# Kernel optimization log

Measured on AMD Instinct MI355X. Metric: run time of the kernel, lower is better.

Reference implementation:

```python
import jax, jax.numpy as jnp
import numpy as np

N_USER = 25000
N_ITEM = 25000
N = N_USER + N_ITEM
E = 1_250_000
D = 64
L = 3
B = 4096


def setup_inputs() -> dict:
    key = jax.random.key(0)
    ks = jax.random.split(key, 11)
    emb = jax.random.normal(ks[0], (N, D), dtype=jnp.float32) * 0.1
    w1_w = jax.random.normal(ks[1], (L, D, D), dtype=jnp.float32) / np.sqrt(D)
    w1_b = jax.random.normal(ks[2], (L, D), dtype=jnp.float32) * 0.01
    w2_w = jax.random.normal(ks[3], (L, D, D), dtype=jnp.float32) / np.sqrt(D)
    w2_b = jax.random.normal(ks[4], (L, D), dtype=jnp.float32) * 0.01
    # normalized-laplacian-like nonneg values
    vals = jax.random.uniform(ks[5], (E,), dtype=jnp.float32) * 0.1
    rows = jax.random.randint(ks[6], (E,), 0, N, dtype=jnp.int32)
    cols = jax.random.randint(ks[7], (E,), 0, N, dtype=jnp.int32)
    user = jax.random.randint(ks[8], (B,), 0, N_USER, dtype=jnp.int32)
    pos = jax.random.randint(ks[9], (B,), 0, N, dtype=jnp.int32)
    neg = jax.random.randint(ks[10], (B,), 0, N, dtype=jnp.int32)
    return {"emb": emb, "w1_w": w1_w, "w1_b": w1_b, "w2_w": w2_w,
            "w2_b": w2_b, "vals": vals, "rows": rows, "cols": cols,
            "user": user, "pos": pos, "neg": neg}


def _spmm(vals, rows, cols, x):
    # sparse [N,N] @ dense [N,D] via gather + segment_sum
    msg = vals[:, None] * x[cols]          # [E, D]
    return jax.ops.segment_sum(msg, rows, num_segments=N)  # [N, D]


def reference(emb, w1_w, w1_b, w2_w, w2_b, vals, rows, cols, user, pos, neg):
    user_embs = [emb[user]]
    pos_embs = [emb[pos]]
    neg_embs = [emb[neg]]
    for l in range(L):
        agg = _spmm(vals, rows, cols, emb)                # sp.mm(laplacian, emb)
        # (laplacian + identity) @ emb == agg + emb
        sx = (agg + emb) @ w1_w[l].T + w1_b[l]
        ox = agg * (emb @ w2_w[l].T + w2_b[l])
        emb = jax.nn.leaky_relu(sx + ox, negative_slope=0.01)
        user_embs.append(emb[user])
        pos_embs.append(emb[pos])
        neg_embs.append(emb[neg])
    user_e = jnp.concatenate(user_embs, axis=-1)          # [B, (L+1)*D]
    pos_e = jnp.concatenate(pos_embs, axis=-1)
    neg_e = jnp.concatenate(neg_embs, axis=-1)
    pos_logits = jnp.einsum('id,id->i', user_e, pos_e)
    neg_logits = jnp.einsum('id,id->i', user_e, neg_e)
    # -log(sigmoid(diff)).sum(), computed stably
    return -jnp.sum(jax.nn.log_sigmoid(pos_logits - neg_logits))
```

## Files before the change

kernel.cpp:

```cpp
#include <hip/hip_runtime.h>
#include <hip/hip_fp16.h>
#include <math.h>

#define N_NODES 50000
#define EDGES   1250000
#define DIM     64
#define NLAYER  3
#define BATCH   4096
#define NSLOTS  (3 * BATCH)

#define NBUCK 196
#define RPB   256
#define NABLK 512
#define CAP_S 7424
#define BCAP  CAP_S
#define PER_BLK ((EDGES + NABLK - 1) / NABLK)

typedef unsigned int uint32;
typedef _Float16 f16x8 __attribute__((ext_vector_type(8)));
typedef float f32x4 __attribute__((ext_vector_type(4)));

static __device__ __forceinline__ ushort f2h(float f) {
    return __half_as_ushort(__float2half(f));
}
static __device__ __forceinline__ float h2f(ushort u) {
    return __half2float(__ushort_as_half(u));
}

static __device__ __forceinline__ int slot_node(int slot,
                                                const int* __restrict__ user,
                                                const int* __restrict__ pos,
                                                const int* __restrict__ neg) {
    if (slot < BATCH) return user[slot];
    if (slot < 2 * BATCH) return pos[slot - BATCH];
    return neg[slot - 2 * BATCH];
}


#define SP_F2H   512
#define SP_DOTS  3637
#define SP_TOTAL 4661

__global__ __launch_bounds__(256) void scatterprep_kernel(const int* __restrict__ rows,
                                                          const int* __restrict__ cols,
                                                          const float* __restrict__ vals,
                                                          int* __restrict__ gcur,
                                                          int2* __restrict__ staging,
                                                          const float* __restrict__ emb,
                                                          ushort* __restrict__ xh,
                                                          const int* __restrict__ user,
                                                          const int* __restrict__ pos,
                                                          const int* __restrict__ neg,
                                                          float* __restrict__ dots,
                                                          float* __restrict__ out) {
    __shared__ int2 sedge[PER_BLK];
    __shared__ int h[NBUCK];
    __shared__ int roff[NBUCK];
    int blk = blockIdx.x;
    int tid = threadIdx.x;
    if (blk < SP_F2H) {
        if (blk == 0 && tid == 0) out[0] = 0.f;
        for (int i = tid; i < NBUCK; i += 256) h[i] = 0;
        __syncthreads();
        int e0 = blk * PER_BLK;
        int e1 = min(e0 + PER_BLK, EDGES);
        int cnt = e1 - e0;
        for (int i = tid; i < cnt; i += 256) {
            int e = e0 + i;
            int r = rows[e];
            sedge[i] = make_int2((r << 16) | cols[e], __float_as_int(vals[e]));
            atomicAdd(&h[r >> 8], 1);
        }
        __syncthreads();
        for (int t = tid; t < NBUCK; t += 256)
            roff[t] = t * CAP_S + atomicAdd(&gcur[t], h[t]);
        __syncthreads();
        for (int i = tid; i < cnt; i += 256) {
            int2 e = sedge[i];
            int bkt = ((uint32)e.x) >> 24;
            int p = atomicAdd(&roff[bkt], 1);
            if (p < (bkt + 1) * CAP_S)
                staging[p] = make_int2(e.x & 0x00FFFFFF, e.y);
        }
    } else if (blk < SP_DOTS) {
        int i = (blk - SP_F2H) * 256 + tid;
        float4 v = ((const float4*)emb)[i];
        ushort4 hh;
        hh.x = f2h(v.x); hh.y = f2h(v.y); hh.z = f2h(v.z); hh.w = f2h(v.w);
        ((ushort4*)xh)[i] = hh;
    } else {
        int lane = tid & 63;
        int i = (blk - SP_DOTS) * 4 + (tid >> 6);
        int ui = user[i], pi = pos[i], ni = neg[i];
        float u = emb[(size_t)ui * DIM + lane];
        float p = emb[(size_t)pi * DIM + lane];
        float n = emb[(size_t)ni * DIM + lane];
        float v = u * (p - n);
#pragma unroll
        for (int off = 32; off; off >>= 1) v += __shfl_xor(v, off);
        if (lane == 0) dots[i] = v;
    }
}


__global__ __launch_bounds__(512) void csr_build_kernel(const int* __restrict__ gcur,
                                                        const int2* __restrict__ staging,
                                                        int* __restrict__ row_ptr,
                                                        uint32* __restrict__ csr) {
    __shared__ int2 sedge[BCAP];
    __shared__ int sbase[256];
    __shared__ int rcur[RPB];
    __shared__ int wred[4];
    int b = blockIdx.x;
    int tid = threadIdx.x;
    int lane = tid & 63, wid = tid >> 6;

    int tot = (tid < NBUCK) ? gcur[tid] : 0;
    int sB = tot;
    if (tid < 256) {
#pragma unroll
        for (int off = 1; off < 64; off <<= 1) {
            int tt = __shfl_up(sB, off);
            if (lane >= off) sB += tt;
        }
        if (lane == 63) wred[wid] = sB;
    }
    __syncthreads();
    if (tid == 0) {
        int a = 0;
#pragma unroll
        for (int i = 0; i < 4; ++i) { int tt = wred[i]; wred[i] = a; a += tt; }
    }
    __syncthreads();
    if (tid < 256) sbase[tid] = wred[wid] + sB - tot;
    __syncthreads();
    int base = sbase[b];
    int cnt = (b == NBUCK - 1) ? (EDGES - sbase[NBUCK - 1]) : (sbase[b + 1] - sbase[b]);
    int sbeg = b * CAP_S;
    __syncthreads();

    if (tid < RPB) rcur[tid] = 0;
    __syncthreads();
    for (int p = tid; p < cnt; p += 512) {
        int2 e = staging[sbeg + p];
        sedge[p] = e;
        atomicAdd(&rcur[e.x >> 16], 1);
    }
    __syncthreads();
    int v = 0, s = 0;
    if (tid < RPB) {
        v = rcur[tid];
        s = v;
#pragma unroll
        for (int off = 1; off < 64; off <<= 1) {
            int t = __shfl_up(s, off);
            if (lane >= off) s += t;
        }
        if (lane == 63) wred[wid] = s;
    }
    __syncthreads();
    if (tid == 0) {
        int a = 0;
#pragma unroll
        for (int i = 0; i < 4; ++i) { int t = wred[i]; wred[i] = a; a += t; }
    }
    __syncthreads();
    if (tid < RPB) {
        int excl = wred[wid] + s - v;
        rcur[tid] = base + excl;
        int row = b * RPB + tid;
        if (row < N_NODES) row_ptr[row] = base + excl;
    }
    if (b == NBUCK - 1 && tid == 0) row_ptr[N_NODES] = EDGES;
    __syncthreads();
    for (int p = tid; p < cnt; p += 512) {
        int2 e = sedge[p];
        int pos = atomicAdd(&rcur[e.x >> 16], 1);
        csr[pos] = ((uint32)(e.x & 0xFFFF) << 16) | (uint32)f2h(__int_as_float(e.y));
    }
}


static __device__ __forceinline__ void spmm_row(const uint32* __restrict__ csr,
                                                const ushort* __restrict__ xh,
                                                int p0, int p1, int g, int sl,
                                                float* a) {
#define SPMM_ACC(E, X)                                                     \
    {                                                                      \
        float vv = h2f((ushort)((E) & 0xFFFF));                            \
        a[0] += vv * h2f((ushort)((X).x & 0xFFFF));                        \
        a[1] += vv * h2f((ushort)((X).x >> 16));                           \
        a[2] += vv * h2f((ushort)((X).y & 0xFFFF));                        \
        a[3] += vv * h2f((ushort)((X).y >> 16));                           \
        a[4] += vv * h2f((ushort)((X).z & 0xFFFF));                        \
        a[5] += vv * h2f((ushort)((X).z >> 16));                           \
        a[6] += vv * h2f((ushort)((X).w & 0xFFFF));                        \
        a[7] += vv * h2f((ushort)((X).w >> 16));                           \
    }
    int p = p0;
    for (; p + 32 <= p1; p += 32) {
        uint32 e0 = csr[p + g];
        uint32 e1 = csr[p + 8 + g];
        uint32 e2 = csr[p + 16 + g];
        uint32 e3 = csr[p + 24 + g];
        uint4 x0 = *(const uint4*)(xh + (size_t)(e0 >> 16) * DIM + sl * 8);
        uint4 x1 = *(const uint4*)(xh + (size_t)(e1 >> 16) * DIM + sl * 8);
        uint4 x2 = *(const uint4*)(xh + (size_t)(e2 >> 16) * DIM + sl * 8);
        uint4 x3 = *(const uint4*)(xh + (size_t)(e3 >> 16) * DIM + sl * 8);
        SPMM_ACC(e0, x0);
        SPMM_ACC(e1, x1);
        SPMM_ACC(e2, x2);
        SPMM_ACC(e3, x3);
    }
    for (; p + 8 <= p1; p += 8) {
        uint32 ea = csr[p + g];
        uint4 xa = *(const uint4*)(xh + (size_t)(ea >> 16) * DIM + sl * 8);
        SPMM_ACC(ea, xa);
    }
    if (p + g < p1) {
        uint32 ea = csr[p + g];
        uint4 xa = *(const uint4*)(xh + (size_t)(ea >> 16) * DIM + sl * 8);
        SPMM_ACC(ea, xa);
    }
#undef SPMM_ACC
#pragma unroll
    for (int m = 8; m <= 32; m <<= 1) {
        a[0] += __shfl_xor(a[0], m); a[1] += __shfl_xor(a[1], m);
        a[2] += __shfl_xor(a[2], m); a[3] += __shfl_xor(a[3], m);
        a[4] += __shfl_xor(a[4], m); a[5] += __shfl_xor(a[5], m);
        a[6] += __shfl_xor(a[6], m); a[7] += __shfl_xor(a[7], m);
    }
}

static __device__ __forceinline__ void spmm_store(ushort* dst, const float* a, int lane) {
    if (lane < 8) {
        ushort t[8];
        t[0] = f2h(a[0]); t[1] = f2h(a[1]); t[2] = f2h(a[2]); t[3] = f2h(a[3]);
        t[4] = f2h(a[4]); t[5] = f2h(a[5]); t[6] = f2h(a[6]); t[7] = f2h(a[7]);
        *(uint4*)(dst + lane * 8) = *(uint4*)t;
    }
}

static __device__ __forceinline__ void dots_tail(const ushort* __restrict__ xh,
                                                 const int* __restrict__ user,
                                                 const int* __restrict__ pos,
                                                 const int* __restrict__ neg,
                                                 float* __restrict__ dots,
                                                 int i, int lane) {
    int ui = user[i], pi = pos[i], ni = neg[i];
    float u = h2f(xh[(size_t)ui * DIM + lane]);
    float p = h2f(xh[(size_t)pi * DIM + lane]);
    float n = h2f(xh[(size_t)ni * DIM + lane]);
    float v = u * (p - n);
#pragma unroll
    for (int off = 32; off; off >>= 1) v += __shfl_xor(v, off);
    if (lane == 0) dots[i] = v;
}


__global__ __launch_bounds__(256) void spmm_kernel(const int* __restrict__ row_ptr,
                                                   const uint32* __restrict__ csr,
                                                   const ushort* __restrict__ xh,
                                                   ushort* __restrict__ aggh,
                                                   const int* __restrict__ user,
                                                   const int* __restrict__ pos,
                                                   const int* __restrict__ neg,
                                                   float* __restrict__ dots,
                                                   int nsb) {
    int lane = threadIdx.x & 63;
    if ((int)blockIdx.x >= nsb) {
        int i = (blockIdx.x - nsb) * 4 + (threadIdx.x >> 6);
        dots_tail(xh, user, pos, neg, dots, i, lane);
        return;
    }
    int row = blockIdx.x * 4 + (threadIdx.x >> 6);
    int p0 = row_ptr[row], p1 = row_ptr[row + 1];
    float a[8] = {};
    spmm_row(csr, xh, p0, p1, lane >> 3, lane & 7, a);
    spmm_store(aggh + (size_t)row * DIM, a, lane);
}


__global__ __launch_bounds__(256) void spmm_slots_kernel(const int* __restrict__ row_ptr,
                                                         const uint32* __restrict__ csr,
                                                         const ushort* __restrict__ xh,
                                                         ushort* __restrict__ aggh_slot,
                                                         const int* __restrict__ user,
                                                         const int* __restrict__ pos,
                                                         const int* __restrict__ neg,
                                                         float* __restrict__ dots,
                                                         int nsb) {
    int lane = threadIdx.x & 63;
    if ((int)blockIdx.x >= nsb) {
        int i = (blockIdx.x - nsb) * 4 + (threadIdx.x >> 6);
        dots_tail(xh, user, pos, neg, dots, i, lane);
        return;
    }
    int slot = blockIdx.x * 4 + (threadIdx.x >> 6);
    int node = slot_node(slot, user, pos, neg);
    int p0 = row_ptr[node], p1 = row_ptr[node + 1];
    float a[8] = {};
    spmm_row(csr, xh, p0, p1, lane >> 3, lane & 7, a);
    spmm_store(aggh_slot + (size_t)slot * DIM, a, lane);
}


template <int IS_SLOT>
static __device__ __forceinline__ void dense_body(const ushort* __restrict__ xh_in,
                                                  const ushort* __restrict__ aggh,
                                                  const float* __restrict__ w1,
                                                  const float* __restrict__ w2,
                                                  const float* __restrict__ b1,
                                                  const float* __restrict__ b2,
                                                  ushort* __restrict__ yh,
                                                  const int* __restrict__ user,
                                                  const int* __restrict__ pos,
                                                  const int* __restrict__ neg) {
    __shared__ ushort xs[64 * 64];
    __shared__ ushort xc[64 * 64];
    __shared__ ushort w1s[64 * 64];
    __shared__ ushort w2s[64 * 64];

    int tid = threadIdx.x;
    int n0 = blockIdx.x * 64;

    {
        int rr = tid >> 2;
        int jq = (tid & 3) << 4;
        int sw = rr & 7;
        int b0 = jq >> 3;
        int o0 = rr * 64 + (((b0 + 0) ^ sw) << 3);
        int o1 = rr * 64 + (((b0 + 1) ^ sw) << 3);

        {
            const float* w1r = w1 + rr * 64 + jq;
            const float* w2r = w2 + rr * 64 + jq;
            ushort t1[16], t2[16];
#pragma unroll
            for (int k = 0; k < 4; ++k) {
                float4 a = ((const float4*)w1r)[k];
                float4 b = ((const float4*)w2r)[k];
                t1[k * 4 + 0] = f2h(a.x); t1[k * 4 + 1] = f2h(a.y);
                t1[k * 4 + 2] = f2h(a.z); t1[k * 4 + 3] = f2h(a.w);
                t2[k * 4 + 0] = f2h(b.x); t2[k * 4 + 1] = f2h(b.y);
                t2[k * 4 + 2] = f2h(b.z); t2[k * 4 + 3] = f2h(b.w);
            }
            *(uint4*)&w1s[o0] = *(uint4*)&t1[0];
            *(uint4*)&w1s[o1] = *(uint4*)&t1[8];
            *(uint4*)&w2s[o0] = *(uint4*)&t2[0];
            *(uint4*)&w2s[o1] = *(uint4*)&t2[8];
        }
        {
            int rowid = n0 + rr;
            int xnode, arow;
            if (IS_SLOT) {
                xnode = slot_node(rowid, user, pos, neg);
                arow = rowid;
            } else {
                xnode = (rowid < N_NODES) ? rowid : (N_NODES - 1);
                arow = xnode;
            }
            const ushort* ar = aggh + (size_t)arow * DIM + jq;
            const ushort* xr = xh_in + (size_t)xnode * DIM + jq;
            ushort txs[16], txc[16];
#pragma unroll
            for (int k = 0; k < 2; ++k) {
                uint4 xv = ((const uint4*)xr)[k];
                uint4 av = ((const uint4*)ar)[k];
                uint32 xw[4] = {xv.x, xv.y, xv.z, xv.w};
                uint32 aw[4] = {av.x, av.y, av.z, av.w};
#pragma unroll
                for (int q = 0; q < 4; ++q) {
                    ushort xlo = (ushort)(xw[q] & 0xFFFF);
                    ushort xhi = (ushort)(xw[q] >> 16);
                    ushort alo = (ushort)(aw[q] & 0xFFFF);
                    ushort ahi = (ushort)(aw[q] >> 16);
                    int e = k * 8 + q * 2;
                    txc[e] = xlo; txc[e + 1] = xhi;
                    txs[e] = f2h(h2f(xlo) + h2f(alo));
                    txs[e + 1] = f2h(h2f(xhi) + h2f(ahi));
                }
            }
            *(uint4*)&xs[o0] = *(uint4*)&txs[0];
            *(uint4*)&xs[o1] = *(uint4*)&txs[8];
            *(uint4*)&xc[o0] = *(uint4*)&txc[0];
            *(uint4*)&xc[o1] = *(uint4*)&txc[8];
        }
    }
    __syncthreads();

    int lane = tid & 63, w = tid >> 6;
    int nb = w << 4;
    int lm = lane & 15;
    int le = lane >> 4;

    f16x8 axs[2], axc[2];
#pragma unroll
    for (int k = 0; k < 2; ++k) {
        int n = nb + lm;
        int blk = k * 4 + le;
        int off = n * 64 + ((blk ^ (n & 7)) << 3);
        axs[k] = *(const f16x8*)&xs[off];
        axc[k] = *(const f16x8*)&xc[off];
    }

#pragma unroll
    for (int dt = 0; dt < 4; ++dt) {
        int d = dt * 16 + lm;
        f16x8 bf1[2], bf2[2];
#pragma unroll
        for (int k = 0; k < 2; ++k) {
            int blk = k * 4 + le;
            int off = d * 64 + ((blk ^ (d & 7)) << 3);
            bf1[k] = *(const f16x8*)&w1s[off];
            bf2[k] = *(const f16x8*)&w2s[off];
        }
        f32x4 acc1 = {0.f, 0.f, 0.f, 0.f};
        f32x4 acc2 = {0.f, 0.f, 0.f, 0.f};
        acc1 = __builtin_amdgcn_mfma_f32_16x16x32_f16(axs[0], bf1[0], acc1, 0, 0, 0);
        acc1 = __builtin_amdgcn_mfma_f32_16x16x32_f16(axs[1], bf1[1], acc1, 0, 0, 0);
        acc2 = __builtin_amdgcn_mfma_f32_16x16x32_f16(axc[0], bf2[0], acc2, 0, 0, 0);
        acc2 = __builtin_amdgcn_mfma_f32_16x16x32_f16(axc[1], bf2[1], acc2, 0, 0, 0);

        float b1v = b1[d], b2v = b2[d];
        int bb = d >> 3;
#pragma unroll
        for (int i = 0; i < 4; ++i) {
            int nl = nb + (le << 2) + i;
            int rowid = n0 + nl;
            int off = nl * 64 + ((bb ^ (nl & 7)) << 3) + (d & 7);
            float ag = h2f(xs[off]) - h2f(xc[off]);
            float t = acc1[i] + b1v + ag * (acc2[i] + b2v);
            t = (t > 0.f) ? t : 0.01f * t;
            bool wr = IS_SLOT ? true : (rowid < N_NODES);
            if (wr) yh[(size_t)rowid * DIM + d] = f2h(t);
        }
    }
}

__global__ __launch_bounds__(256) void dense_kernel(const ushort* __restrict__ xh_in,
                                                    const ushort* __restrict__ aggh,
                                                    const float* __restrict__ w1,
                                                    const float* __restrict__ w2,
                                                    const float* __restrict__ b1,
                                                    const float* __restrict__ b2,
                                                    ushort* __restrict__ yh) {
    dense_body<0>(xh_in, aggh, w1, w2, b1, b2, yh, nullptr, nullptr, nullptr);
}

__global__ __launch_bounds__(256) void dense_slots_kernel(const ushort* __restrict__ xh_in,
                                                          const ushort* __restrict__ aggh_slot,
                                                          const float* __restrict__ w1,
                                                          const float* __restrict__ w2,
                                                          const float* __restrict__ b1,
                                                          const float* __restrict__ b2,
                                                          ushort* __restrict__ yh_slot,
                                                          const int* __restrict__ user,
                                                          const int* __restrict__ pos,
                                                          const int* __restrict__ neg) {
    dense_body<1>(xh_in, aggh_slot, w1, w2, b1, b2, yh_slot, user, pos, neg);
}


__global__ __launch_bounds__(256) void dots_loss_kernel(const ushort* __restrict__ yh_slot,
                                                        const float* __restrict__ dots,
                                                        float* __restrict__ out) {
    __shared__ float part[4];
    int tid = threadIdx.x;
    int lane = tid & 63;
    int i = blockIdx.x * 4 + (tid >> 6);
    float u = h2f(yh_slot[(size_t)i * DIM + lane]);
    float p = h2f(yh_slot[(size_t)(BATCH + i) * DIM + lane]);
    float n = h2f(yh_slot[(size_t)(2 * BATCH + i) * DIM + lane]);
    float v = u * (p - n);
#pragma unroll
    for (int off = 32; off; off >>= 1) v += __shfl_xor(v, off);
    if (lane == 0) {
        float d = dots[i] + dots[BATCH + i] + dots[2 * BATCH + i] + v;
        part[tid >> 6] = fmaxf(-d, 0.f) + log1pf(expf(-fabsf(d)));
    }
    __syncthreads();
    if (tid == 0) atomicAdd(out, part[0] + part[1] + part[2] + part[3]);
}


extern "C" void kernel_launch(void* const* d_in, const int* in_sizes, int n_in,
                              void* d_out, int out_size, void* d_ws, size_t ws_size,
                              hipStream_t stream) {
    const float* emb  = (const float*)d_in[0];
    const float* w1_w = (const float*)d_in[1];
    const float* w1_b = (const float*)d_in[2];
    const float* w2_w = (const float*)d_in[3];
    const float* w2_b = (const float*)d_in[4];
    const float* vals = (const float*)d_in[5];
    const int* rows = (const int*)d_in[6];
    const int* cols = (const int*)d_in[7];
    const int* user = (const int*)d_in[8];
    const int* pos  = (const int*)d_in[9];
    const int* neg  = (const int*)d_in[10];
    float* out = (float*)d_out;

    char* w = (char*)d_ws;
    char* region = w;          w += (size_t)NBUCK * CAP_S * 8;
    ushort* aggh = (ushort*)region;
    int2* staging = (int2*)region;
    int* row_ptr = (int*)w;   w += (((size_t)(N_NODES + 1) * 4) + 255) / 256 * 256;
    uint32* csr  = (uint32*)w; w += (size_t)EDGES * 4;
    int* gcur    = (int*)w;   w += 256 * 4;
    float* dots  = (float*)w; w += (size_t)3 * BATCH * 4;
    ushort* xhA  = (ushort*)w; w += (size_t)N_NODES * DIM * 2;
    ushort* xhB  = (ushort*)w; w += (size_t)N_NODES * DIM * 2;
    ushort* aggh_slot = (ushort*)w; w += (size_t)NSLOTS * DIM * 2;
    ushort* yh_slot   = (ushort*)w; w += (size_t)NSLOTS * DIM * 2;

    hipMemsetAsync(gcur, 0, 256 * 4, stream);

    scatterprep_kernel<<<SP_TOTAL, 256, 0, stream>>>(rows, cols, vals, gcur, staging,
                                                     emb, xhA, user, pos, neg, dots, out);
    csr_build_kernel<<<NBUCK, 512, 0, stream>>>(gcur, staging, row_ptr, csr);

    const int NSB = N_NODES / 4;
    const int NTB = BATCH / 4;
    const int NDB = (N_NODES + 63) / 64;
    const int NSLB = NSLOTS / 4;
    const int NSDB = NSLOTS / 64;

    spmm_kernel<<<NSB, 256, 0, stream>>>(row_ptr, csr, xhA, aggh, user, pos, neg, dots, NSB);
    dense_kernel<<<NDB, 256, 0, stream>>>(xhA, aggh, w1_w + 0 * 4096, w2_w + 0 * 4096,
                                          w1_b + 0 * DIM, w2_b + 0 * DIM, xhB);
    spmm_kernel<<<NSB + NTB, 256, 0, stream>>>(row_ptr, csr, xhB, aggh, user, pos, neg,
                                               dots + BATCH, NSB);
    dense_kernel<<<NDB, 256, 0, stream>>>(xhB, aggh, w1_w + 1 * 4096, w2_w + 1 * 4096,
                                          w1_b + 1 * DIM, w2_b + 1 * DIM, xhA);
    spmm_slots_kernel<<<NSLB + NTB, 256, 0, stream>>>(row_ptr, csr, xhA, aggh_slot,
                                                      user, pos, neg, dots + 2 * BATCH, NSLB);
    dense_slots_kernel<<<NSDB, 256, 0, stream>>>(xhA, aggh_slot,
                                                 w1_w + 2 * 4096, w2_w + 2 * 4096,
                                                 w1_b + 2 * DIM, w2_b + 2 * DIM,
                                                 yh_slot, user, pos, neg);

    dots_loss_kernel<<<NTB, 256, 0, stream>>>(yh_slot, dots, out);
}
```

Measured before the change: 150.3 us.

## Store node embeddings as int8 with per-row scales instead of fp16

Switches the inter-layer embedding buffers from fp16 to int8 with one float scale per row, cutting the bytes gathered per edge in the SpMM in half. Dequantisation multiplies by a per-column scale load inside the inner loop, and the dense stage now computes a per-row absmax through shuffles and writes quantised bytes. This adds extra scale loads, conversion arithmetic and narrower byte stores, and it lowers numerical precision, which may hurt accuracy tolerance.

```diff
diff --git a/kernel.cpp b/kernel.cpp
--- a/kernel.cpp
+++ b/kernel.cpp
@@ -25,6 +25,14 @@
 }
 static __device__ __forceinline__ float h2f(ushort u) {
     return __half2float(__ushort_as_half(u));
+}
+static __device__ __forceinline__ float b2f(uint32 w, int k) {
+    return (float)(int)(char)(w >> (8 * k));
+}
+static __device__ __forceinline__ char fq(float v, float inv_scale) {
+    float q = rintf(v * inv_scale);
+    q = fminf(fmaxf(q, -127.f), 127.f);
+    return (char)(int)q;
 }
 
 static __device__ __forceinline__ int slot_node(int slot,
@@ -37,9 +45,9 @@
 }
 
 
-#define SP_F2H   512
-#define SP_DOTS  3637
-#define SP_TOTAL 4661
+#define SP_QNT   512
+#define SP_DOTS  13012
+#define SP_TOTAL 14036
 
 __global__ __launch_bounds__(256) void scatterprep_kernel(const int* __restrict__ rows,
                                                           const int* __restrict__ cols,
@@ -47,7 +55,8 @@
                                                           int* __restrict__ gcur,
                                                           int2* __restrict__ staging,
                                                           const float* __restrict__ emb,
-                                                          ushort* __restrict__ xh,
+                                                          char* __restrict__ xq,
+                                                          float* __restrict__ xscale,
                                                           const int* __restrict__ user,
                                                           const int* __restrict__ pos,
                                                           const int* __restrict__ neg,
@@ -58,7 +67,7 @@
     __shared__ int roff[NBUCK];
     int blk = blockIdx.x;
     int tid = threadIdx.x;
-    if (blk < SP_F2H) {
+    if (blk < SP_QNT) {
         if (blk == 0 && tid == 0) out[0] = 0.f;
         for (int i = tid; i < NBUCK; i += 256) h[i] = 0;
         __syncthreads();
@@ -83,11 +92,15 @@
                 staging[p] = make_int2(e.x & 0x00FFFFFF, e.y);
         }
     } else if (blk < SP_DOTS) {
-        int i = (blk - SP_F2H) * 256 + tid;
-        float4 v = ((const float4*)emb)[i];
-        ushort4 hh;
-        hh.x = f2h(v.x); hh.y = f2h(v.y); hh.z = f2h(v.z); hh.w = f2h(v.w);
-        ((ushort4*)xh)[i] = hh;
+        int lane = tid & 63;
+        int row = (blk - SP_QNT) * 4 + (tid >> 6);
+        float v = emb[(size_t)row * DIM + lane];
+        float m = fabsf(v);
+#pragma unroll
+        for (int off = 32; off; off >>= 1) m = fmaxf(m, __shfl_xor(m, off));
+        float scale = fmaxf(m, 1e-8f) * (1.f / 127.f);
+        xq[(size_t)row * DIM + lane] = fq(v, 127.f / fmaxf(m, 1e-8f));
+        if (lane == 0) xscale[row] = scale;
     } else {
         int lane = tid & 63;
         int i = (blk - SP_DOTS) * 4 + (tid >> 6);
@@ -182,20 +195,22 @@
 
 
 static __device__ __forceinline__ void spmm_row(const uint32* __restrict__ csr,
-                                                const ushort* __restrict__ xh,
+                                                const char* __restrict__ xq,
+                                                const float* __restrict__ xscale,
                                                 int p0, int p1, int g, int sl,
                                                 float* a) {
 #define SPMM_ACC(E, X)                                                     \
     {                                                                      \
-        float vv = h2f((ushort)((E) & 0xFFFF));                            \
-        a[0] += vv * h2f((ushort)((X).x & 0xFFFF));                        \
-        a[1] += vv * h2f((ushort)((X).x >> 16));                           \
-        a[2] += vv * h2f((ushort)((X).y & 0xFFFF));                        \
-        a[3] += vv * h2f((ushort)((X).y >> 16));                           \
-        a[4] += vv * h2f((ushort)((X).z & 0xFFFF));                        \
-        a[5] += vv * h2f((ushort)((X).z >> 16));                           \
-        a[6] += vv * h2f((ushort)((X).w & 0xFFFF));                        \
-        a[7] += vv * h2f((ushort)((X).w >> 16));                           \
+        int c_ = (E) >> 16;                                                \
+        float vv = h2f((ushort)((E) & 0xFFFF)) * xscale[c_];               \
+        a[0] += vv * b2f((X).x, 0);                                        \
+        a[1] += vv * b2f((X).x, 1);                                        \
+        a[2] += vv * b2f((X).x, 2);                                        \
+        a[3] += vv * b2f((X).x, 3);                                        \
+        a[4] += vv * b2f((X).y, 0);                                        \
+        a[5] += vv * b2f((X).y, 1);                                        \
+        a[6] += vv * b2f((X).y, 2);                                        \
+        a[7] += vv * b2f((X).y, 3);                                        \
     }
     int p = p0;
     for (; p + 32 <= p1; p += 32) {
@@ -203,10 +218,10 @@
         uint32 e1 = csr[p + 8 + g];
         uint32 e2 = csr[p + 16 + g];
         uint32 e3 = csr[p + 24 + g];
-        uint4 x0 = *(const uint4*)(xh + (size_t)(e0 >> 16) * DIM + sl * 8);
-        uint4 x1 = *(const uint4*)(xh + (size_t)(e1 >> 16) * DIM + sl * 8);
-        uint4 x2 = *(const uint4*)(xh + (size_t)(e2 >> 16) * DIM + sl * 8);
-        uint4 x3 = *(const uint4*)(xh + (size_t)(e3 >> 16) * DIM + sl * 8);
+        uint2 x0 = *(const uint2*)(xq + (size_t)(e0 >> 16) * DIM + sl * 8);
+        uint2 x1 = *(const uint2*)(xq + (size_t)(e1 >> 16) * DIM + sl * 8);
+        uint2 x2 = *(const uint2*)(xq + (size_t)(e2 >> 16) * DIM + sl * 8);
+        uint2 x3 = *(const uint2*)(xq + (size_t)(e3 >> 16) * DIM + sl * 8);
         SPMM_ACC(e0, x0);
         SPMM_ACC(e1, x1);
         SPMM_ACC(e2, x2);
@@ -214,12 +229,12 @@
     }
     for (; p + 8 <= p1; p += 8) {
         uint32 ea = csr[p + g];
-        uint4 xa = *(const uint4*)(xh + (size_t)(ea >> 16) * DIM + sl * 8);
+        uint2 xa = *(const uint2*)(xq + (size_t)(ea >> 16) * DIM + sl * 8);
         SPMM_ACC(ea, xa);
     }
     if (p + g < p1) {
         uint32 ea = csr[p + g];
-        uint4 xa = *(const uint4*)(xh + (size_t)(ea >> 16) * DIM + sl * 8);
+        uint2 xa = *(const uint2*)(xq + (size_t)(ea >> 16) * DIM + sl * 8);
         SPMM_ACC(ea, xa);
     }
 #undef SPMM_ACC
@@ -241,16 +256,17 @@
     }
 }
 
-static __device__ __forceinline__ void dots_tail(const ushort* __restrict__ xh,
-                                                 const int* __restrict__ user,
-                                                 const int* __restrict__ pos,
-                                                 const int* __restrict__ neg,
-                                                 float* __restrict__ dots,
-                                                 int i, int lane) {
+static __device__ __forceinline__ void dots_tail_q(const char* __restrict__ xq,
+                                                   const float* __restrict__ xscale,
+                                                   const int* __restrict__ user,
+                                                   const int* __restrict__ pos,
+                                                   const int* __restrict__ neg,
+                                                   float* __restrict__ dots,
+                                                   int i, int lane) {
     int ui = user[i], pi = pos[i], ni = neg[i];
-    float u = h2f(xh[(size_t)ui * DIM + lane]);
-    float p = h2f(xh[(size_t)pi * DIM + lane]);
-    float n = h2f(xh[(size_t)ni * DIM + lane]);
+    float u = (float)(int)xq[(size_t)ui * DIM + lane] * xscale[ui];
+    float p = (float)(int)xq[(size_t)pi * DIM + lane] * xscale[pi];
+    float n = (float)(int)xq[(size_t)ni * DIM + lane] * xscale[ni];
     float v = u * (p - n);
 #pragma unroll
     for (int off = 32; off; off >>= 1) v += __shfl_xor(v, off);
@@ -260,7 +276,8 @@
 
 __global__ __launch_bounds__(256) void spmm_kernel(const int* __restrict__ row_ptr,
                                                    const uint32* __restrict__ csr,
-                                                   const ushort* __restrict__ xh,
+                                                   const char* __restrict__ xq,
+                                                   const float* __restrict__ xscale,
                                                    ushort* __restrict__ aggh,
                                                    const int* __restrict__ user,
                                                    const int* __restrict__ pos,
@@ -270,20 +287,21 @@
     int lane = threadIdx.x & 63;
     if ((int)blockIdx.x >= nsb) {
         int i = (blockIdx.x - nsb) * 4 + (threadIdx.x >> 6);
-        dots_tail(xh, user, pos, neg, dots, i, lane);
+        dots_tail_q(xq, xscale, user, pos, neg, dots, i, lane);
         return;
     }
     int row = blockIdx.x * 4 + (threadIdx.x >> 6);
     int p0 = row_ptr[row], p1 = row_ptr[row + 1];
     float a[8] = {};
-    spmm_row(csr, xh, p0, p1, lane >> 3, lane & 7, a);
+    spmm_row(csr, xq, xscale, p0, p1, lane >> 3, lane & 7, a);
     spmm_store(aggh + (size_t)row * DIM, a, lane);
 }
 
 
 __global__ __launch_bounds__(256) void spmm_slots_kernel(const int* __restrict__ row_ptr,
                                                          const uint32* __restrict__ csr,
-                                                         const ushort* __restrict__ xh,
+                                                         const char* __restrict__ xq,
+                                                         const float* __restrict__ xscale,
                                                          ushort* __restrict__ aggh_slot,
                                                          const int* __restrict__ user,
                                                          const int* __restrict__ pos,
@@ -293,26 +311,28 @@
     int lane = threadIdx.x & 63;
     if ((int)blockIdx.x >= nsb) {
         int i = (blockIdx.x - nsb) * 4 + (threadIdx.x >> 6);
-        dots_tail(xh, user, pos, neg, dots, i, lane);
+        dots_tail_q(xq, xscale, user, pos, neg, dots, i, lane);
         return;
     }
     int slot = blockIdx.x * 4 + (threadIdx.x >> 6);
     int node = slot_node(slot, user, pos, neg);
     int p0 = row_ptr[node], p1 = row_ptr[node + 1];
     float a[8] = {};
-    spmm_row(csr, xh, p0, p1, lane >> 3, lane & 7, a);
+    spmm_row(csr, xq, xscale, p0, p1, lane >> 3, lane & 7, a);
     spmm_store(aggh_slot + (size_t)slot * DIM, a, lane);
 }
 
 
 template <int IS_SLOT>
-static __device__ __forceinline__ void dense_body(const ushort* __restrict__ xh_in,
+static __device__ __forceinline__ void dense_body(const char* __restrict__ xq_in,
+                                                  const float* __restrict__ xscale_in,
                                                   const ushort* __restrict__ aggh,
                                                   const float* __restrict__ w1,
                                                   const float* __restrict__ w2,
                                                   const float* __restrict__ b1,
                                                   const float* __restrict__ b2,
-                                                  ushort* __restrict__ yh,
+                                                  char* __restrict__ yq,
+                                                  float* __restrict__ yscale,
                                                   const int* __restrict__ user,
                                                   const int* __restrict__ pos,
                                                   const int* __restrict__ neg) {
@@ -360,25 +380,19 @@
                 xnode = (rowid < N_NODES) ? rowid : (N_NODES - 1);
                 arow = xnode;
             }
+            float xsc = xscale_in[xnode];
             const ushort* ar = aggh + (size_t)arow * DIM + jq;
-            const ushort* xr = xh_in + (size_t)xnode * DIM + jq;
+            uint4 qv = *(const uint4*)(xq_in + (size_t)xnode * DIM + jq);
+            uint32 qw[4] = {qv.x, qv.y, qv.z, qv.w};
             ushort txs[16], txc[16];
 #pragma unroll
-            for (int k = 0; k < 2; ++k) {
-                uint4 xv = ((const uint4*)xr)[k];
-                uint4 av = ((const uint4*)ar)[k];
-                uint32 xw[4] = {xv.x, xv.y, xv.z, xv.w};
-                uint32 aw[4] = {av.x, av.y, av.z, av.w};
-#pragma unroll
-                for (int q = 0; q < 4; ++q) {
-                    ushort xlo = (ushort)(xw[q] & 0xFFFF);
-                    ushort xhi = (ushort)(xw[q] >> 16);
-                    ushort alo = (ushort)(aw[q] & 0xFFFF);
-                    ushort ahi = (ushort)(aw[q] >> 16);
-                    int e = k * 8 + q * 2;
-                    txc[e] = xlo; txc[e + 1] = xhi;
-                    txs[e] = f2h(h2f(xlo) + h2f(alo));
-                    txs[e + 1] = f2h(h2f(xhi) + h2f(ahi));
+            for (int q = 0; q < 4; ++q) {
+#pragma unroll
+                for (int k = 0; k < 4; ++k) {
+                    int e = q * 4 + k;
+                    float xv = b2f(qw[q], k) * xsc;
+                    txc[e] = f2h(xv);
+                    txs[e] = f2h(xv + h2f(ar[e]));
                 }
             }
             *(uint4*)&xs[o0] = *(uint4*)&txs[0];
@@ -404,6 +418,8 @@
         axc[k] = *(const f16x8*)&xc[off];
     }
 
+    float tv[4][4];
+
 #pragma unroll
     for (int dt = 0; dt < 4; ++dt) {
         int d = dt * 16 + lm;
@@ -427,51 +443,77 @@
 #pragma unroll
         for (int i = 0; i < 4; ++i) {
             int nl = nb + (le << 2) + i;
-            int rowid = n0 + nl;
             int off = nl * 64 + ((bb ^ (nl & 7)) << 3) + (d & 7);
             float ag = h2f(xs[off]) - h2f(xc[off]);
             float t = acc1[i] + b1v + ag * (acc2[i] + b2v);
-            t = (t > 0.f) ? t : 0.01f * t;
-            bool wr = IS_SLOT ? true : (rowid < N_NODES);
-            if (wr) yh[(size_t)rowid * DIM + d] = f2h(t);
-        }
-    }
-}
-
-__global__ __launch_bounds__(256) void dense_kernel(const ushort* __restrict__ xh_in,
+            tv[dt][i] = (t > 0.f) ? t : 0.01f * t;
+        }
+    }
+
+#pragma unroll
+    for (int i = 0; i < 4; ++i) {
+        int nl = nb + (le << 2) + i;
+        int rowid = n0 + nl;
+        float m = fmaxf(fmaxf(fabsf(tv[0][i]), fabsf(tv[1][i])),
+                        fmaxf(fabsf(tv[2][i]), fabsf(tv[3][i])));
+#pragma unroll
+        for (int off = 1; off < 16; off <<= 1) m = fmaxf(m, __shfl_xor(m, off));
+        float mm = fmaxf(m, 1e-8f);
+        float inv = 127.f / mm;
+        bool wr = IS_SLOT ? true : (rowid < N_NODES);
+        if (wr) {
+            if (lm == 0) yscale[rowid] = mm * (1.f / 127.f);
+#pragma unroll
+            for (int dt = 0; dt < 4; ++dt)
+                yq[(size_t)rowid * DIM + dt * 16 + lm] = fq(tv[dt][i], inv);
+        }
+    }
+}
+
+__global__ __launch_bounds__(256) void dense_kernel(const char* __restrict__ xq_in,
+                                                    const float* __restrict__ xscale_in,
                                                     const ushort* __restrict__ aggh,
                                                     const float* __restrict__ w1,
                                                     const float* __restrict__ w2,
                                                     const float* __restrict__ b1,
                                                     const float* __restrict__ b2,
-                                                    ushort* __restrict__ yh) {
-    dense_body<0>(xh_in, aggh, w1, w2, b1, b2, yh, nullptr, nullptr, nullptr);
-}
-
-__global__ __launch_bounds__(256) void dense_slots_kernel(const ushort* __restrict__ xh_in,
+                                                    char* __restrict__ yq,
+                                                    float* __restrict__ yscale) {
+    dense_body<0>(xq_in, xscale_in, aggh, w1, w2, b1, b2, yq, yscale,
+                  nullptr, nullptr, nullptr);
+}
+
+__global__ __launch_bounds__(256) void dense_slots_kernel(const char* __restrict__ xq_in,
+                                                          const float* __restrict__ xscale_in,
                                                           const ushort* __restrict__ aggh_slot,
                                                           const float* __restrict__ w1,
                                                           const float* __restrict__ w2,
                                                           const float* __restrict__ b1,
                                                           const float* __restrict__ b2,
-                                                          ushort* __restrict__ yh_slot,
+                                                          char* __restrict__ yq_slot,
+                                                          float* __restrict__ yscale_slot,
                                                           const int* __restrict__ user,
                                                           const int* __restrict__ pos,
                                                           const int* __restrict__ neg) {
-    dense_body<1>(xh_in, aggh_slot, w1, w2, b1, b2, yh_slot, user, pos, neg);
-}
-
-
-__global__ __launch_bounds__(256) void dots_loss_kernel(const ushort* __restrict__ yh_slot,
+    dense_body<1>(xq_in, xscale_in, aggh_slot, w1, w2, b1, b2, yq_slot, yscale_slot,
+                  user, pos, neg);
+}
+
+
+__global__ __launch_bounds__(256) void dots_loss_kernel(const char* __restrict__ yq_slot,
+                                                        const float* __restrict__ yscale_slot,
                                                         const float* __restrict__ dots,
                                                         float* __restrict__ out) {
     __shared__ float part[4];
     int tid = threadIdx.x;
     int lane = tid & 63;
     int i = blockIdx.x * 4 + (tid >> 6);
-    float u = h2f(yh_slot[(size_t)i * DIM + lane]);
-    float p = h2f(yh_slot[(size_t)(BATCH + i) * DIM + lane]);
-    float n = h2f(yh_slot[(size_t)(2 * BATCH + i) * DIM + lane]);
+    float su = yscale_slot[i];
+    float sp = yscale_slot[BATCH + i];
+    float sn = yscale_slot[2 * BATCH + i];
+    float u = (float)(int)yq_slot[(size_t)i * DIM + lane] * su;
+    float p = (float)(int)yq_slot[(size_t)(BATCH + i) * DIM + lane] * sp;
+    float n = (float)(int)yq_slot[(size_t)(2 * BATCH + i) * DIM + lane] * sn;
     float v = u * (p - n);
 #pragma unroll
     for (int off = 32; off; off >>= 1) v += __shfl_xor(v, off);
@@ -508,15 +550,19 @@
     uint32* csr  = (uint32*)w; w += (size_t)EDGES * 4;
     int* gcur    = (int*)w;   w += 256 * 4;
     float* dots  = (float*)w; w += (size_t)3 * BATCH * 4;
-    ushort* xhA  = (ushort*)w; w += (size_t)N_NODES * DIM * 2;
-    ushort* xhB  = (ushort*)w; w += (size_t)N_NODES * DIM * 2;
+    char* xqA    = (char*)w;  w += (size_t)N_NODES * DIM;
+    char* xqB    = (char*)w;  w += (size_t)N_NODES * DIM;
+    float* xscA  = (float*)w; w += (size_t)N_NODES * 4;
+    float* xscB  = (float*)w; w += (size_t)N_NODES * 4;
     ushort* aggh_slot = (ushort*)w; w += (size_t)NSLOTS * DIM * 2;
-    ushort* yh_slot   = (ushort*)w; w += (size_t)NSLOTS * DIM * 2;
+    char* yq_slot     = (char*)w;   w += (size_t)NSLOTS * DIM;
+    float* ysc_slot   = (float*)w;  w += (size_t)NSLOTS * 4;
 
     hipMemsetAsync(gcur, 0, 256 * 4, stream);
 
     scatterprep_kernel<<<SP_TOTAL, 256, 0, stream>>>(rows, cols, vals, gcur, staging,
-                                                     emb, xhA, user, pos, neg, dots, out);
+                                                     emb, xqA, xscA,
+                                                     user, pos, neg, dots, out);
     csr_build_kernel<<<NBUCK, 512, 0, stream>>>(gcur, staging, row_ptr, csr);
 
     const int NSB = N_NODES / 4;
@@ -525,19 +571,22 @@
     const int NSLB = NSLOTS / 4;
     const int NSDB = NSLOTS / 64;
 
-    spmm_kernel<<<NSB, 256, 0, stream>>>(row_ptr, csr, xhA, aggh, user, pos, neg, dots, NSB);
-    dense_kernel<<<NDB, 256, 0, stream>>>(xhA, aggh, w1_w + 0 * 4096, w2_w + 0 * 4096,
-                                          w1_b + 0 * DIM, w2_b + 0 * DIM, xhB);
-    spmm_kernel<<<NSB + NTB, 256, 0, stream>>>(row_ptr, csr, xhB, aggh, user, pos, neg,
-                                               dots + BATCH, NSB);
-    dense_kernel<<<NDB, 256, 0, stream>>>(xhB, aggh, w1_w + 1 * 4096, w2_w + 1 * 4096,
-                                          w1_b + 1 * DIM, w2_b + 1 * DIM, xhA);
-    spmm_slots_kernel<<<NSLB + NTB, 256, 0, stream>>>(row_ptr, csr, xhA, aggh_slot,
+    spmm_kernel<<<NSB, 256, 0, stream>>>(row_ptr, csr, xqA, xscA, aggh,
+                                         user, pos, neg, dots, NSB);
+    dense_kernel<<<NDB, 256, 0, stream>>>(xqA, xscA, aggh,
+                                          w1_w + 0 * 4096, w2_w + 0 * 4096,
+                                          w1_b + 0 * DIM, w2_b + 0 * DIM, xqB, xscB);
+    spmm_kernel<<<NSB + NTB, 256, 0, stream>>>(row_ptr, csr, xqB, xscB, aggh,
+                                               user, pos, neg, dots + BATCH, NSB);
+    dense_kernel<<<NDB, 256, 0, stream>>>(xqB, xscB, aggh,
+                                          w1_w + 1 * 4096, w2_w + 1 * 4096,
+                                          w1_b + 1 * DIM, w2_b + 1 * DIM, xqA, xscA);
+    spmm_slots_kernel<<<NSLB + NTB, 256, 0, stream>>>(row_ptr, csr, xqA, xscA, aggh_slot,
                                                       user, pos, neg, dots + 2 * BATCH, NSLB);
-    dense_slots_kernel<<<NSDB, 256, 0, stream>>>(xhA, aggh_slot,
+    dense_slots_kernel<<<NSDB, 256, 0, stream>>>(xqA, xscA, aggh_slot,
                                                  w1_w + 2 * 4096, w2_w + 2 * 4096,
                                                  w1_b + 2 * DIM, w2_b + 2 * DIM,
-                                                 yh_slot, user, pos, neg);
-
-    dots_loss_kernel<<<NTB, 256, 0, stream>>>(yh_slot, dots, out);
-}
+                                                 yq_slot, ysc_slot, user, pos, neg);
+
+    dots_loss_kernel<<<NTB, 256, 0, stream>>>(yq_slot, ysc_slot, dots, out);
+}
```

New measurement: 144.0 us. 4.2% less time.
